# Performance work log

Measured on AMD Instinct MI355X. Metric: run time of the kernel, lower is better.

## Reference

```python
import jax, jax.numpy as jnp
import numpy as np

D = 1024      # config.input_dim
H = 16        # config.num_heads
EPS = 1e-6    # layernorm epsilon


def setup_inputs() -> dict:
    key = jax.random.key(0)
    ks = jax.random.split(key, 12)
    B, S = 4, 2048
    s = 1.0 / np.sqrt(D)
    return {
        "Q": jax.random.normal(ks[0], (B, S, D), jnp.float32),
        "K": jax.random.normal(ks[1], (B, S, D), jnp.float32),
        "V": jax.random.normal(ks[2], (B, S, D), jnp.float32),
        "Wq": jax.random.normal(ks[3], (D, D), jnp.float32) * s,
        "bq": jnp.zeros((D,), jnp.float32),
        "Wk": jax.random.normal(ks[4], (D, D), jnp.float32) * s,
        "bk": jnp.zeros((D,), jnp.float32),
        "Wv": jax.random.normal(ks[5], (D, D), jnp.float32) * s,
        "bv": jnp.zeros((D,), jnp.float32),
        "Wo": jax.random.normal(ks[6], (D, D), jnp.float32) * s,
        "bo": jnp.zeros((D,), jnp.float32),
        "gamma": jnp.ones((D,), jnp.float32),
        "beta": jnp.zeros((D,), jnp.float32),
    }


def _layernorm(x, gamma, beta):
    mu = jnp.mean(x, axis=-1, keepdims=True)
    var = jnp.mean(jnp.square(x - mu), axis=-1, keepdims=True)
    return (x - mu) * jax.lax.rsqrt(var + EPS) * gamma + beta


def reference(Q, K, V, Wq, bq, Wk, bk, Wv, bv, Wo, bo, gamma, beta):
    # Type == 'D': pre-norm projections, causal MHA (no 1/sqrt(d) scaling,
    # faithful to source), out projection, residual. Dropout = identity (eval).
    B, S, _ = Q.shape
    dh = D // H
    clone_Q = Q
    q = _layernorm(Q, gamma, beta) @ Wq + bq
    k = _layernorm(K, gamma, beta) @ Wk + bk
    v = _layernorm(V, gamma, beta) @ Wv + bv
    # [B, S, D] -> [B, H, S, dh]
    q = q.reshape(B, S, H, dh).transpose(0, 2, 1, 3)
    k = k.reshape(B, S, H, dh).transpose(0, 2, 1, 3)
    v = v.reshape(B, S, H, dh).transpose(0, 2, 1, 3)
    score = jnp.einsum("bhsd,bhtd->bhst", q, k)  # [B, H, S, S]
    causal = jnp.tril(jnp.ones((S, S), bool))
    score = jnp.where(causal, score, -jnp.inf)
    attn = jax.nn.softmax(score, axis=-1)
    out = jnp.einsum("bhst,bhtd->bhsd", attn, v)  # [B, H, S, dh]
    out = out.transpose(0, 2, 1, 3).reshape(B, S, D)
    return clone_Q + (out @ Wo + bo)
```

## Files before the change

kernel.cpp:

```cpp
#include <hip/hip_runtime.h>
#include <hip/hip_bf16.h>

typedef __attribute__((ext_vector_type(8))) __bf16 bf16x8;
typedef __attribute__((ext_vector_type(4))) float f32x4;

union BF8U { uint4 u; bf16x8 b; };

static __device__ __forceinline__ unsigned short f2bf(float f){
  union { float f; unsigned int u; } a; a.f = f;
  unsigned int u = a.u;
  return (unsigned short)((u + 0x7fffu + ((u >> 16) & 1u)) >> 16);
}

static __device__ __forceinline__ bf16x8 ld_bf8(const unsigned short* p){
  BF8U u; u.u = *reinterpret_cast<const uint4*>(p); return u.b;
}

static __device__ __forceinline__ f32x4 mfma16(bf16x8 a, bf16x8 b, f32x4 c){
  return __builtin_amdgcn_mfma_f32_16x16x32_bf16(a, b, c, 0, 0, 0);
}

static __device__ __forceinline__ void gl_lds16(const unsigned short* g, unsigned short* l){
  __builtin_amdgcn_global_load_lds(
      (const __attribute__((address_space(1))) unsigned int*)g,
      (__attribute__((address_space(3))) unsigned int*)l, 16, 0, 0);
}

__global__ __launch_bounds__(256) void ln_kernel(const float* __restrict__ X,
    const float* __restrict__ gamma, const float* __restrict__ beta,
    unsigned short* __restrict__ out)
{
  const int row = blockIdx.x;
  const int t = threadIdx.x;
  const float4 x = reinterpret_cast<const float4*>(X + (size_t)row*1024)[t];
  float s  = x.x + x.y + x.z + x.w;
  float ss = x.x*x.x + x.y*x.y + x.z*x.z + x.w*x.w;
  for (int off = 1; off < 64; off <<= 1){
    s  += __shfl_xor(s, off);
    ss += __shfl_xor(ss, off);
  }
  __shared__ float red[8];
  const int wv = t >> 6;
  if ((t & 63) == 0){ red[wv] = s; red[4 + wv] = ss; }
  __syncthreads();
  s  = red[0] + red[1] + red[2] + red[3];
  ss = red[4] + red[5] + red[6] + red[7];
  const float mu   = s * (1.0f/1024.0f);
  const float var  = ss * (1.0f/1024.0f) - mu*mu;
  const float rstd = rsqrtf(var + 1e-6f);
  const float4 gm = reinterpret_cast<const float4*>(gamma)[t];
  const float4 bt = reinterpret_cast<const float4*>(beta)[t];
  unsigned short pk[4];
  pk[0] = f2bf((x.x - mu)*rstd*gm.x + bt.x);
  pk[1] = f2bf((x.y - mu)*rstd*gm.y + bt.y);
  pk[2] = f2bf((x.z - mu)*rstd*gm.z + bt.z);
  pk[3] = f2bf((x.w - mu)*rstd*gm.w + bt.w);
  *reinterpret_cast<uint2*>(out + (size_t)row*1024 + t*4) = *reinterpret_cast<uint2*>(pk);
}

__global__ __launch_bounds__(256) void wt_kernel(const float* __restrict__ W,
    unsigned short* __restrict__ Wt)
{
  __shared__ unsigned short tile[64][72];
  const int t = threadIdx.x;
  const int bk = ((int)blockIdx.x >> 4) * 64;
  const int bn = ((int)blockIdx.x & 15) * 64;
  {
    const int kr = t >> 2, nc0 = (t & 3) * 16;
    const float4* src = reinterpret_cast<const float4*>(W + (size_t)(bk + kr)*1024 + bn + nc0);
    for (int q = 0; q < 4; ++q){
      float4 vv = src[q];
      tile[kr][nc0 + q*4 + 0] = f2bf(vv.x);
      tile[kr][nc0 + q*4 + 1] = f2bf(vv.y);
      tile[kr][nc0 + q*4 + 2] = f2bf(vv.z);
      tile[kr][nc0 + q*4 + 3] = f2bf(vv.w);
    }
  }
  __syncthreads();
  {
    const int nr = t >> 2, kc0 = (t & 3) * 16;
    unsigned short outv[16];
    for (int j = 0; j < 16; ++j) outv[j] = tile[kc0 + j][nr];
    uint4* dst = reinterpret_cast<uint4*>(Wt + (size_t)(bn + nr)*1024 + bk + kc0);
    dst[0] = reinterpret_cast<uint4*>(outv)[0];
    dst[1] = reinterpret_cast<uint4*>(outv)[1];
  }
}

template<int MODE>
__global__ __launch_bounds__(256) void gemm_kernel(
    const unsigned short* __restrict__ A,
    const unsigned short* __restrict__ Bt,
    const float* __restrict__ bias,
    const float* __restrict__ residual,
    unsigned short* __restrict__ outb,
    float* __restrict__ outf)
{
  __shared__ unsigned short a_lds[128][64];
  __shared__ unsigned short b_lds[128][64];
  const int t = threadIdx.x;
  const int lane = t & 63;
  const int w = t >> 6;
  const int g = lane >> 4, c = lane & 15;
  const int bm = (int)blockIdx.x >> 3, bn = (int)blockIdx.x & 7;
  const int wr = w >> 1, wc = w & 1;
  const int row0 = bm * 128, col0 = bn * 128;

  f32x4 acc[4][4];
  const f32x4 fz = {0.f, 0.f, 0.f, 0.f};
  for (int i = 0; i < 4; ++i) for (int j = 0; j < 4; ++j) acc[i][j] = fz;

  for (int kb = 0; kb < 1024; kb += 64){
    for (int i = 0; i < 4; ++i){
      const int cid = t + i*256;
      const int r = cid >> 3, ch = cid & 7;
      const int chs = (ch ^ (r & 7)) * 8;
      gl_lds16(&A [(size_t)(row0 + r)*1024 + kb + chs], &a_lds[0][0] + cid*8);
      gl_lds16(&Bt[(size_t)(col0 + r)*1024 + kb + chs], &b_lds[0][0] + cid*8);
    }
    __syncthreads();
    bf16x8 af[4][2], bfr[4][2];
    for (int mt = 0; mt < 4; ++mt)
      for (int kc = 0; kc < 2; ++kc){
        const int R = wr*64 + mt*16 + c;
        af[mt][kc] = ld_bf8(&a_lds[R][((kc*4 + g) ^ (R & 7))*8]);
      }
    for (int nt = 0; nt < 4; ++nt)
      for (int kc = 0; kc < 2; ++kc){
        const int R = wc*64 + nt*16 + c;
        bfr[nt][kc] = ld_bf8(&b_lds[R][((kc*4 + g) ^ (R & 7))*8]);
      }
    for (int kc = 0; kc < 2; ++kc)
      for (int mt = 0; mt < 4; ++mt)
        for (int nt = 0; nt < 4; ++nt)
          acc[mt][nt] = mfma16(af[mt][kc], bfr[nt][kc], acc[mt][nt]);
    __syncthreads();
  }

  for (int mt = 0; mt < 4; ++mt){
    for (int nt = 0; nt < 4; ++nt){
      const int gcol = col0 + wc*64 + nt*16 + c;
      const float bv = bias[gcol];
      if (MODE == 2){
        const int grow0 = row0 + wr*64 + mt*16 + g*4;
        const int bidx = grow0 >> 11, s0 = grow0 & 2047;
        const int hh = gcol >> 6, d = gcol & 63;
        unsigned short pk[4];
        for (int r = 0; r < 4; ++r) pk[r] = f2bf(acc[mt][nt][r] + bv);
        *reinterpret_cast<uint2*>(&outb[((size_t)((bidx*16 + hh)*64 + d))*2048 + s0]) =
          *reinterpret_cast<uint2*>(pk);
      } else {
        for (int r = 0; r < 4; ++r){
          const int grow = row0 + wr*64 + mt*16 + g*4 + r;
          float v = acc[mt][nt][r] + bv;
          if (MODE == 0){
            const int bidx = grow >> 11, s = grow & 2047;
            const int hh = gcol >> 6, d = gcol & 63;
            outb[((size_t)(bidx*16 + hh)*2048 + s)*64 + d] = f2bf(v);
          } else {
            const size_t idx = (size_t)grow*1024 + gcol;
            outf[idx] = v + residual[idx];
          }
        }
      }
    }
  }
}

__global__ __launch_bounds__(256) void attn_kernel(
    const unsigned short* __restrict__ qg,
    const unsigned short* __restrict__ kg,
    const unsigned short* __restrict__ vtg,
    unsigned short* __restrict__ og)
{
  __shared__ unsigned short k_lds[64][64];
  __shared__ unsigned short vt_lds[64][64];
  __shared__ unsigned short p_lds[4][32][72];
  const int t = threadIdx.x;
  const int lane = t & 63;
  const int w = t >> 6;
  const int g = lane >> 4, c = lane & 15;
  const int bh = (int)blockIdx.x & 63;
  const int p  = (int)blockIdx.x >> 6;
  const size_t base = (size_t)bh * 2048 * 64;
  const int bidx = bh >> 4, hh = bh & 15;
  const float NEG = -__builtin_inff();
  const f32x4 fz = {0.f,0.f,0.f,0.f};

  for (int half = 0; half < 2; ++half){
    const int qb = half ? (15 - p) : p;
    const int qw = qb*128 + w*32;

    bf16x8 qf[2][2];
    for (int mi = 0; mi < 2; ++mi)
      for (int kc = 0; kc < 2; ++kc)
        qf[mi][kc] = ld_bf8(&qg[base + (size_t)(qw + mi*16 + c)*64 + kc*32 + g*8]);

    f32x4 o_acc[4][2];
    for (int i = 0; i < 4; ++i) for (int j = 0; j < 2; ++j) o_acc[i][j] = fz;
    float m_run[2] = {NEG, NEG};
    float l_run[2] = {0.f, 0.f};

    const int nkv = qb*2 + 2;
    for (int kvt = 0; kvt < nkv; ++kvt){
      const int kv0 = kvt * 64;
      for (int i = 0; i < 2; ++i){
        const int cid = t + i*256;
        const int r = cid >> 3, ch = cid & 7;
        const int chs = (ch ^ (r & 7)) * 8;
        gl_lds16(&kg [base + (size_t)(kv0 + r)*64 + chs], &k_lds[0][0]  + cid*8);
        gl_lds16(&vtg[base + (size_t)r*2048 + kv0 + chs], &vt_lds[0][0] + cid*8);
      }
      __syncthreads();

      if (kv0 <= qw + 31){
        bf16x8 kf[4][2];
        for (int ni = 0; ni < 4; ++ni)
          for (int kc = 0; kc < 2; ++kc){
            const int R = ni*16 + c;
            kf[ni][kc] = ld_bf8(&k_lds[R][((kc*4 + g) ^ (R & 7))*8]);
          }
        f32x4 st[4][2];
        for (int i = 0; i < 4; ++i) for (int j = 0; j < 2; ++j) st[i][j] = fz;
        __builtin_amdgcn_s_setprio(1);
        for (int kc = 0; kc < 2; ++kc)
          for (int ni = 0; ni < 4; ++ni)
            for (int mi = 0; mi < 2; ++mi)
              st[ni][mi] = mfma16(kf[ni][kc], qf[mi][kc], st[ni][mi]);
        __builtin_amdgcn_s_setprio(0);

        const bool need_mask = (kv0 + 63 > qw);
        for (int mi = 0; mi < 2; ++mi){
          const int qglob = qw + mi*16 + c;
          float tmax = NEG;
          if (need_mask){
            for (int ni = 0; ni < 4; ++ni)
              for (int r = 0; r < 4; ++r){
                const int kvglob = kv0 + ni*16 + g*4 + r;
                float sv = (kvglob <= qglob) ? st[ni][mi][r] : NEG;
                st[ni][mi][r] = sv;
                tmax = fmaxf(tmax, sv);
              }
          } else {
            for (int ni = 0; ni < 4; ++ni)
              for (int r = 0; r < 4; ++r)
                tmax = fmaxf(tmax, st[ni][mi][r]);
          }
          tmax = fmaxf(tmax, __shfl_xor(tmax, 16));
          tmax = fmaxf(tmax, __shfl_xor(tmax, 32));
          const float m_new = fmaxf(m_run[mi], tmax);
          const float alpha = __expf(m_run[mi] - m_new);
          float tsum = 0.f;
          for (int ni = 0; ni < 4; ++ni)
            for (int r = 0; r < 4; ++r){
              const float pe = __expf(st[ni][mi][r] - m_new);
              st[ni][mi][r] = pe;
              tsum += pe;
            }
          tsum += __shfl_xor(tsum, 16);
          tsum += __shfl_xor(tsum, 32);
          l_run[mi] = l_run[mi]*alpha + tsum;
          m_run[mi] = m_new;
          for (int ni = 0; ni < 4; ++ni){
            o_acc[ni][mi][0] *= alpha; o_acc[ni][mi][1] *= alpha;
            o_acc[ni][mi][2] *= alpha; o_acc[ni][mi][3] *= alpha;
          }
          for (int ni = 0; ni < 4; ++ni){
            unsigned short pk[4];
            pk[0] = f2bf(st[ni][mi][0]); pk[1] = f2bf(st[ni][mi][1]);
            pk[2] = f2bf(st[ni][mi][2]); pk[3] = f2bf(st[ni][mi][3]);
            *reinterpret_cast<uint2*>(&p_lds[w][mi*16 + c][ni*16 + g*4]) =
              *reinterpret_cast<uint2*>(pk);
          }
        }

        bf16x8 vf[4][2], pf[2][2];
        for (int ni = 0; ni < 4; ++ni)
          for (int kc = 0; kc < 2; ++kc){
            const int R = ni*16 + c;
            vf[ni][kc] = ld_bf8(&vt_lds[R][((kc*4 + g) ^ (R & 7))*8]);
          }
        for (int kc = 0; kc < 2; ++kc)
          for (int mi = 0; mi < 2; ++mi)
            pf[kc][mi] = ld_bf8(&p_lds[w][mi*16 + c][kc*32 + g*8]);
        __builtin_amdgcn_s_setprio(1);
        for (int kc = 0; kc < 2; ++kc)
          for (int ni = 0; ni < 4; ++ni)
            for (int mi = 0; mi < 2; ++mi)
              o_acc[ni][mi] = mfma16(vf[ni][kc], pf[kc][mi], o_acc[ni][mi]);
        __builtin_amdgcn_s_setprio(0);
      }
      __syncthreads();
    }

    for (int mi = 0; mi < 2; ++mi){
      const float invl = 1.0f / l_run[mi];
      const int s = qw + mi*16 + c;
      const size_t obase = ((size_t)(bidx*2048 + s))*1024 + hh*64;
      for (int ni = 0; ni < 4; ++ni){
        unsigned short pk[4];
        pk[0] = f2bf(o_acc[ni][mi][0]*invl);
        pk[1] = f2bf(o_acc[ni][mi][1]*invl);
        pk[2] = f2bf(o_acc[ni][mi][2]*invl);
        pk[3] = f2bf(o_acc[ni][mi][3]*invl);
        *reinterpret_cast<uint2*>(&og[obase + ni*16 + g*4]) =
          *reinterpret_cast<uint2*>(pk);
      }
    }
  }
}

extern "C" void kernel_launch(void* const* d_in, const int* in_sizes, int n_in,
                              void* d_out, int out_size, void* d_ws, size_t ws_size,
                              hipStream_t stream)
{
  (void)in_sizes; (void)n_in; (void)out_size;
  const float* Q  = (const float*)d_in[0];
  const float* K  = (const float*)d_in[1];
  const float* V  = (const float*)d_in[2];
  const float* Wq = (const float*)d_in[3];
  const float* bq = (const float*)d_in[4];
  const float* Wk = (const float*)d_in[5];
  const float* bk = (const float*)d_in[6];
  const float* Wv = (const float*)d_in[7];
  const float* bv = (const float*)d_in[8];
  const float* Wo = (const float*)d_in[9];
  const float* bo = (const float*)d_in[10];
  const float* gamma = (const float*)d_in[11];
  const float* beta  = (const float*)d_in[12];

  const size_t MB = 1024ull*1024ull;
  if (ws_size < 104*MB) return;
  char* ws = (char*)d_ws;
  unsigned short* lnQ = (unsigned short*)(ws + 0*MB);
  unsigned short* lnK = (unsigned short*)(ws + 16*MB);
  unsigned short* lnV = (unsigned short*)(ws + 32*MB);
  unsigned short* attn_out = lnQ;
  unsigned short* WtQ = (unsigned short*)(ws + 48*MB);
  unsigned short* WtK = (unsigned short*)(ws + 50*MB);
  unsigned short* WtV = (unsigned short*)(ws + 52*MB);
  unsigned short* WtO = (unsigned short*)(ws + 54*MB);
  unsigned short* qb  = (unsigned short*)(ws + 56*MB);
  unsigned short* kb  = (unsigned short*)(ws + 72*MB);
  unsigned short* vtb = (unsigned short*)(ws + 88*MB);
  float* out = (float*)d_out;

  wt_kernel<<<256, 256, 0, stream>>>(Wq, WtQ);
  wt_kernel<<<256, 256, 0, stream>>>(Wk, WtK);
  wt_kernel<<<256, 256, 0, stream>>>(Wv, WtV);
  wt_kernel<<<256, 256, 0, stream>>>(Wo, WtO);
  ln_kernel<<<8192, 256, 0, stream>>>(Q, gamma, beta, lnQ);
  ln_kernel<<<8192, 256, 0, stream>>>(K, gamma, beta, lnK);
  ln_kernel<<<8192, 256, 0, stream>>>(V, gamma, beta, lnV);
  gemm_kernel<0><<<512, 256, 0, stream>>>(lnQ, WtQ, bq, nullptr, qb,  nullptr);
  gemm_kernel<0><<<512, 256, 0, stream>>>(lnK, WtK, bk, nullptr, kb,  nullptr);
  gemm_kernel<2><<<512, 256, 0, stream>>>(lnV, WtV, bv, nullptr, vtb, nullptr);
  attn_kernel<<<512, 256, 0, stream>>>(qb, kb, vtb, attn_out);
  gemm_kernel<1><<<512, 256, 0, stream>>>(attn_out, WtO, bo, Q, nullptr, out);
}
```

Measured before the change: 378.3 us.

## Merge prep and QKV launches, retile attention to 8 waves with deferred rescale

Folds the three layernorm launches and four weight transposes into one prep kernel, and the three QKV projections into a single 1536-block GEMM launch. The goal is to cut launch overhead and fill the GPU better. Attention moves to 512-thread blocks where each wave owns 16 query rows instead of 32, which reduces register pressure. Softmax pre-scales Q by log2(e) to use exp2, and skips the running-max rescale while the max grows by no more than a threshold. f2bf becomes a native cast. Deferring the rescale allows larger exponents before overflow, and halving each wave's query rows loses some K/V fragment reuse per wave.

Result: faster. 336.9 us (-10.9%).

```diff
diff --git a/kernel.cpp b/kernel.cpp
--- a/kernel.cpp
+++ b/kernel.cpp
@@ -7,9 +7,8 @@
 union BF8U { uint4 u; bf16x8 b; };
 
 static __device__ __forceinline__ unsigned short f2bf(float f){
-  union { float f; unsigned int u; } a; a.f = f;
-  unsigned int u = a.u;
-  return (unsigned short)((u + 0x7fffu + ((u >> 16) & 1u)) >> 16);
+  __bf16 h = (__bf16)f;
+  return *reinterpret_cast<unsigned short*>(&h);
 }
 
 static __device__ __forceinline__ bf16x8 ld_bf8(const unsigned short* p){
@@ -26,74 +25,168 @@
       (__attribute__((address_space(3))) unsigned int*)l, 16, 0, 0);
 }
 
-__global__ __launch_bounds__(256) void ln_kernel(const float* __restrict__ X,
+__global__ __launch_bounds__(256) void prep_kernel(
+    const float* __restrict__ Q, const float* __restrict__ K, const float* __restrict__ V,
     const float* __restrict__ gamma, const float* __restrict__ beta,
-    unsigned short* __restrict__ out)
+    unsigned short* __restrict__ lnQ, unsigned short* __restrict__ lnK,
+    unsigned short* __restrict__ lnV,
+    const float* __restrict__ Wq, const float* __restrict__ Wk,
+    const float* __restrict__ Wv, const float* __restrict__ Wo,
+    unsigned short* __restrict__ WtQ, unsigned short* __restrict__ WtK,
+    unsigned short* __restrict__ WtV, unsigned short* __restrict__ WtO)
 {
-  const int row = blockIdx.x;
+  __shared__ __align__(16) unsigned short smem[64*72];
+  const int bid = (int)blockIdx.x;
   const int t = threadIdx.x;
-  const float4 x = reinterpret_cast<const float4*>(X + (size_t)row*1024)[t];
-  float s  = x.x + x.y + x.z + x.w;
-  float ss = x.x*x.x + x.y*x.y + x.z*x.z + x.w*x.w;
-  for (int off = 1; off < 64; off <<= 1){
-    s  += __shfl_xor(s, off);
-    ss += __shfl_xor(ss, off);
-  }
-  __shared__ float red[8];
-  const int wv = t >> 6;
-  if ((t & 63) == 0){ red[wv] = s; red[4 + wv] = ss; }
-  __syncthreads();
-  s  = red[0] + red[1] + red[2] + red[3];
-  ss = red[4] + red[5] + red[6] + red[7];
-  const float mu   = s * (1.0f/1024.0f);
-  const float var  = ss * (1.0f/1024.0f) - mu*mu;
-  const float rstd = rsqrtf(var + 1e-6f);
-  const float4 gm = reinterpret_cast<const float4*>(gamma)[t];
-  const float4 bt = reinterpret_cast<const float4*>(beta)[t];
-  unsigned short pk[4];
-  pk[0] = f2bf((x.x - mu)*rstd*gm.x + bt.x);
-  pk[1] = f2bf((x.y - mu)*rstd*gm.y + bt.y);
-  pk[2] = f2bf((x.z - mu)*rstd*gm.z + bt.z);
-  pk[3] = f2bf((x.w - mu)*rstd*gm.w + bt.w);
-  *reinterpret_cast<uint2*>(out + (size_t)row*1024 + t*4) = *reinterpret_cast<uint2*>(pk);
-}
-
-__global__ __launch_bounds__(256) void wt_kernel(const float* __restrict__ W,
-    unsigned short* __restrict__ Wt)
+  if (bid < 24576){
+    const int sel = bid >> 13;
+    const int row = bid & 8191;
+    const float* X = sel==0 ? Q : sel==1 ? K : V;
+    unsigned short* out = sel==0 ? lnQ : sel==1 ? lnK : lnV;
+    float* red = reinterpret_cast<float*>(smem);
+    const float4 x = reinterpret_cast<const float4*>(X + (size_t)row*1024)[t];
+    float s  = x.x + x.y + x.z + x.w;
+    float ss = x.x*x.x + x.y*x.y + x.z*x.z + x.w*x.w;
+    for (int off = 1; off < 64; off <<= 1){
+      s  += __shfl_xor(s, off);
+      ss += __shfl_xor(ss, off);
+    }
+    const int wv = t >> 6;
+    if ((t & 63) == 0){ red[wv] = s; red[4 + wv] = ss; }
+    __syncthreads();
+    s  = red[0] + red[1] + red[2] + red[3];
+    ss = red[4] + red[5] + red[6] + red[7];
+    const float mu   = s * (1.0f/1024.0f);
+    const float var  = ss * (1.0f/1024.0f) - mu*mu;
+    const float rstd = rsqrtf(var + 1e-6f);
+    const float4 gm = reinterpret_cast<const float4*>(gamma)[t];
+    const float4 bt = reinterpret_cast<const float4*>(beta)[t];
+    unsigned short pk[4];
+    pk[0] = f2bf((x.x - mu)*rstd*gm.x + bt.x);
+    pk[1] = f2bf((x.y - mu)*rstd*gm.y + bt.y);
+    pk[2] = f2bf((x.z - mu)*rstd*gm.z + bt.z);
+    pk[3] = f2bf((x.w - mu)*rstd*gm.w + bt.w);
+    *reinterpret_cast<uint2*>(out + (size_t)row*1024 + t*4) = *reinterpret_cast<uint2*>(pk);
+  } else {
+    const int wid = bid - 24576;
+    const int wsel = wid >> 8;
+    const float* W = wsel==0 ? Wq : wsel==1 ? Wk : wsel==2 ? Wv : Wo;
+    unsigned short* Wt = wsel==0 ? WtQ : wsel==1 ? WtK : wsel==2 ? WtV : WtO;
+    unsigned short (*tile)[72] = reinterpret_cast<unsigned short(*)[72]>(smem);
+    const int tb = wid & 255;
+    const int bk = (tb >> 4) * 64;
+    const int bn = (tb & 15) * 64;
+    {
+      const int kr = t >> 2, nc0 = (t & 3) * 16;
+      const float4* src = reinterpret_cast<const float4*>(W + (size_t)(bk + kr)*1024 + bn + nc0);
+      for (int q = 0; q < 4; ++q){
+        float4 vv = src[q];
+        tile[kr][nc0 + q*4 + 0] = f2bf(vv.x);
+        tile[kr][nc0 + q*4 + 1] = f2bf(vv.y);
+        tile[kr][nc0 + q*4 + 2] = f2bf(vv.z);
+        tile[kr][nc0 + q*4 + 3] = f2bf(vv.w);
+      }
+    }
+    __syncthreads();
+    {
+      const int nr = t >> 2, kc0 = (t & 3) * 16;
+      unsigned short outv[16];
+      for (int j = 0; j < 16; ++j) outv[j] = tile[kc0 + j][nr];
+      uint4* dst = reinterpret_cast<uint4*>(Wt + (size_t)(bn + nr)*1024 + bk + kc0);
+      dst[0] = reinterpret_cast<uint4*>(outv)[0];
+      dst[1] = reinterpret_cast<uint4*>(outv)[1];
+    }
+  }
+}
+
+__global__ __launch_bounds__(256) void qkv_kernel(
+    const unsigned short* __restrict__ lnQ, const unsigned short* __restrict__ lnK,
+    const unsigned short* __restrict__ lnV,
+    const unsigned short* __restrict__ WtQ, const unsigned short* __restrict__ WtK,
+    const unsigned short* __restrict__ WtV,
+    const float* __restrict__ bq, const float* __restrict__ bk,
+    const float* __restrict__ bv,
+    unsigned short* __restrict__ qb, unsigned short* __restrict__ kb,
+    unsigned short* __restrict__ vtb)
 {
-  __shared__ unsigned short tile[64][72];
+  __shared__ unsigned short a_lds[128][64];
+  __shared__ unsigned short b_lds[128][64];
+  const int bid = (int)blockIdx.x;
+  const int which = bid >> 9;
+  const int inner = bid & 511;
+  const unsigned short* A  = which==0 ? lnQ : which==1 ? lnK : lnV;
+  const unsigned short* Bt = which==0 ? WtQ : which==1 ? WtK : WtV;
+  const float* bias = which==0 ? bq : which==1 ? bk : bv;
+
   const int t = threadIdx.x;
-  const int bk = ((int)blockIdx.x >> 4) * 64;
-  const int bn = ((int)blockIdx.x & 15) * 64;
-  {
-    const int kr = t >> 2, nc0 = (t & 3) * 16;
-    const float4* src = reinterpret_cast<const float4*>(W + (size_t)(bk + kr)*1024 + bn + nc0);
-    for (int q = 0; q < 4; ++q){
-      float4 vv = src[q];
-      tile[kr][nc0 + q*4 + 0] = f2bf(vv.x);
-      tile[kr][nc0 + q*4 + 1] = f2bf(vv.y);
-      tile[kr][nc0 + q*4 + 2] = f2bf(vv.z);
-      tile[kr][nc0 + q*4 + 3] = f2bf(vv.w);
-    }
-  }
-  __syncthreads();
-  {
-    const int nr = t >> 2, kc0 = (t & 3) * 16;
-    unsigned short outv[16];
-    for (int j = 0; j < 16; ++j) outv[j] = tile[kc0 + j][nr];
-    uint4* dst = reinterpret_cast<uint4*>(Wt + (size_t)(bn + nr)*1024 + bk + kc0);
-    dst[0] = reinterpret_cast<uint4*>(outv)[0];
-    dst[1] = reinterpret_cast<uint4*>(outv)[1];
-  }
-}
-
-template<int MODE>
-__global__ __launch_bounds__(256) void gemm_kernel(
+  const int lane = t & 63;
+  const int w = t >> 6;
+  const int g = lane >> 4, c = lane & 15;
+  const int bm = inner >> 3, bn = inner & 7;
+  const int wr = w >> 1, wc = w & 1;
+  const int row0 = bm * 128, col0 = bn * 128;
+
+  f32x4 acc[4][4];
+  const f32x4 fz = {0.f, 0.f, 0.f, 0.f};
+  for (int i = 0; i < 4; ++i) for (int j = 0; j < 4; ++j) acc[i][j] = fz;
+
+  for (int kb_ = 0; kb_ < 1024; kb_ += 64){
+    for (int i = 0; i < 4; ++i){
+      const int cid = t + i*256;
+      const int r = cid >> 3, ch = cid & 7;
+      const int chs = (ch ^ (r & 7)) * 8;
+      gl_lds16(&A [(size_t)(row0 + r)*1024 + kb_ + chs], &a_lds[0][0] + cid*8);
+      gl_lds16(&Bt[(size_t)(col0 + r)*1024 + kb_ + chs], &b_lds[0][0] + cid*8);
+    }
+    __syncthreads();
+    bf16x8 af[4][2], bfr[4][2];
+    for (int mt = 0; mt < 4; ++mt)
+      for (int kc = 0; kc < 2; ++kc){
+        const int R = wr*64 + mt*16 + c;
+        af[mt][kc] = ld_bf8(&a_lds[R][((kc*4 + g) ^ (R & 7))*8]);
+      }
+    for (int nt = 0; nt < 4; ++nt)
+      for (int kc = 0; kc < 2; ++kc){
+        const int R = wc*64 + nt*16 + c;
+        bfr[nt][kc] = ld_bf8(&b_lds[R][((kc*4 + g) ^ (R & 7))*8]);
+      }
+    for (int kc = 0; kc < 2; ++kc)
+      for (int mt = 0; mt < 4; ++mt)
+        for (int nt = 0; nt < 4; ++nt)
+          acc[mt][nt] = mfma16(af[mt][kc], bfr[nt][kc], acc[mt][nt]);
+    __syncthreads();
+  }
+
+  const float scale = (which == 0) ? 1.4426950408889634f : 1.0f;
+  unsigned short* outb = which==0 ? qb : kb;
+  for (int mt = 0; mt < 4; ++mt){
+    for (int nt = 0; nt < 4; ++nt){
+      const int gcol = col0 + wc*64 + nt*16 + c;
+      const float bv_ = bias[gcol];
+      const int hh = gcol >> 6, d = gcol & 63;
+      if (which == 2){
+        const int grow0 = row0 + wr*64 + mt*16 + g*4;
+        const int bidx = grow0 >> 11, s0 = grow0 & 2047;
+        unsigned short pk[4];
+        for (int r = 0; r < 4; ++r) pk[r] = f2bf(acc[mt][nt][r] + bv_);
+        *reinterpret_cast<uint2*>(&vtb[((size_t)((bidx*16 + hh)*64 + d))*2048 + s0]) =
+          *reinterpret_cast<uint2*>(pk);
+      } else {
+        for (int r = 0; r < 4; ++r){
+          const int grow = row0 + wr*64 + mt*16 + g*4 + r;
+          const int bidx = grow >> 11, s = grow & 2047;
+          outb[((size_t)(bidx*16 + hh)*2048 + s)*64 + d] = f2bf((acc[mt][nt][r] + bv_)*scale);
+        }
+      }
+    }
+  }
+}
+
+__global__ __launch_bounds__(256) void ogemm_kernel(
     const unsigned short* __restrict__ A,
     const unsigned short* __restrict__ Bt,
     const float* __restrict__ bias,
     const float* __restrict__ residual,
-    unsigned short* __restrict__ outb,
     float* __restrict__ outf)
 {
   __shared__ unsigned short a_lds[128][64];
@@ -110,13 +203,13 @@
   const f32x4 fz = {0.f, 0.f, 0.f, 0.f};
   for (int i = 0; i < 4; ++i) for (int j = 0; j < 4; ++j) acc[i][j] = fz;
 
-  for (int kb = 0; kb < 1024; kb += 64){
+  for (int kb_ = 0; kb_ < 1024; kb_ += 64){
     for (int i = 0; i < 4; ++i){
       const int cid = t + i*256;
       const int r = cid >> 3, ch = cid & 7;
       const int chs = (ch ^ (r & 7)) * 8;
-      gl_lds16(&A [(size_t)(row0 + r)*1024 + kb + chs], &a_lds[0][0] + cid*8);
-      gl_lds16(&Bt[(size_t)(col0 + r)*1024 + kb + chs], &b_lds[0][0] + cid*8);
+      gl_lds16(&A [(size_t)(row0 + r)*1024 + kb_ + chs], &a_lds[0][0] + cid*8);
+      gl_lds16(&Bt[(size_t)(col0 + r)*1024 + kb_ + chs], &b_lds[0][0] + cid*8);
     }
     __syncthreads();
     bf16x8 af[4][2], bfr[4][2];
@@ -140,34 +233,17 @@
   for (int mt = 0; mt < 4; ++mt){
     for (int nt = 0; nt < 4; ++nt){
       const int gcol = col0 + wc*64 + nt*16 + c;
-      const float bv = bias[gcol];
-      if (MODE == 2){
-        const int grow0 = row0 + wr*64 + mt*16 + g*4;
-        const int bidx = grow0 >> 11, s0 = grow0 & 2047;
-        const int hh = gcol >> 6, d = gcol & 63;
-        unsigned short pk[4];
-        for (int r = 0; r < 4; ++r) pk[r] = f2bf(acc[mt][nt][r] + bv);
-        *reinterpret_cast<uint2*>(&outb[((size_t)((bidx*16 + hh)*64 + d))*2048 + s0]) =
-          *reinterpret_cast<uint2*>(pk);
-      } else {
-        for (int r = 0; r < 4; ++r){
-          const int grow = row0 + wr*64 + mt*16 + g*4 + r;
-          float v = acc[mt][nt][r] + bv;
-          if (MODE == 0){
-            const int bidx = grow >> 11, s = grow & 2047;
-            const int hh = gcol >> 6, d = gcol & 63;
-            outb[((size_t)(bidx*16 + hh)*2048 + s)*64 + d] = f2bf(v);
-          } else {
-            const size_t idx = (size_t)grow*1024 + gcol;
-            outf[idx] = v + residual[idx];
-          }
-        }
-      }
-    }
-  }
-}
-
-__global__ __launch_bounds__(256) void attn_kernel(
+      const float bv_ = bias[gcol];
+      for (int r = 0; r < 4; ++r){
+        const int grow = row0 + wr*64 + mt*16 + g*4 + r;
+        const size_t idx = (size_t)grow*1024 + gcol;
+        outf[idx] = acc[mt][nt][r] + bv_ + residual[idx];
+      }
+    }
+  }
+}
+
+__global__ __launch_bounds__(512, 4) void attn_kernel(
     const unsigned short* __restrict__ qg,
     const unsigned short* __restrict__ kg,
     const unsigned short* __restrict__ vtg,
@@ -175,7 +251,7 @@
 {
   __shared__ unsigned short k_lds[64][64];
   __shared__ unsigned short vt_lds[64][64];
-  __shared__ unsigned short p_lds[4][32][72];
+  __shared__ unsigned short p_lds[8][16][72];
   const int t = threadIdx.x;
   const int lane = t & 63;
   const int w = t >> 6;
@@ -187,125 +263,115 @@
   const float NEG = -__builtin_inff();
   const f32x4 fz = {0.f,0.f,0.f,0.f};
 
+  const int sr = t >> 3, sch = t & 7;
+  const int schs = (sch ^ (sr & 7)) * 8;
+
   for (int half = 0; half < 2; ++half){
-    const int qb = half ? (15 - p) : p;
-    const int qw = qb*128 + w*32;
-
-    bf16x8 qf[2][2];
-    for (int mi = 0; mi < 2; ++mi)
-      for (int kc = 0; kc < 2; ++kc)
-        qf[mi][kc] = ld_bf8(&qg[base + (size_t)(qw + mi*16 + c)*64 + kc*32 + g*8]);
-
-    f32x4 o_acc[4][2];
-    for (int i = 0; i < 4; ++i) for (int j = 0; j < 2; ++j) o_acc[i][j] = fz;
-    float m_run[2] = {NEG, NEG};
-    float l_run[2] = {0.f, 0.f};
-
-    const int nkv = qb*2 + 2;
+    const int qb_ = half ? (15 - p) : p;
+    const int qw = qb_*128 + w*16;
+
+    bf16x8 qf[2];
+    for (int kc = 0; kc < 2; ++kc)
+      qf[kc] = ld_bf8(&qg[base + (size_t)(qw + c)*64 + kc*32 + g*8]);
+
+    f32x4 o_acc[4];
+    for (int i = 0; i < 4; ++i) o_acc[i] = fz;
+    float m_run = NEG, l_run = 0.f;
+
+    const int nkv = qb_*2 + 2;
     for (int kvt = 0; kvt < nkv; ++kvt){
       const int kv0 = kvt * 64;
-      for (int i = 0; i < 2; ++i){
-        const int cid = t + i*256;
-        const int r = cid >> 3, ch = cid & 7;
-        const int chs = (ch ^ (r & 7)) * 8;
-        gl_lds16(&kg [base + (size_t)(kv0 + r)*64 + chs], &k_lds[0][0]  + cid*8);
-        gl_lds16(&vtg[base + (size_t)r*2048 + kv0 + chs], &vt_lds[0][0] + cid*8);
-      }
+      gl_lds16(&kg [base + (size_t)(kv0 + sr)*64 + schs], &k_lds[0][0]  + t*8);
+      gl_lds16(&vtg[base + (size_t)sr*2048 + kv0 + schs], &vt_lds[0][0] + t*8);
       __syncthreads();
 
-      if (kv0 <= qw + 31){
+      if (kv0 <= qw + 15){
         bf16x8 kf[4][2];
         for (int ni = 0; ni < 4; ++ni)
           for (int kc = 0; kc < 2; ++kc){
             const int R = ni*16 + c;
             kf[ni][kc] = ld_bf8(&k_lds[R][((kc*4 + g) ^ (R & 7))*8]);
           }
-        f32x4 st[4][2];
-        for (int i = 0; i < 4; ++i) for (int j = 0; j < 2; ++j) st[i][j] = fz;
+        f32x4 st[4];
+        for (int i = 0; i < 4; ++i) st[i] = fz;
         __builtin_amdgcn_s_setprio(1);
         for (int kc = 0; kc < 2; ++kc)
           for (int ni = 0; ni < 4; ++ni)
-            for (int mi = 0; mi < 2; ++mi)
-              st[ni][mi] = mfma16(kf[ni][kc], qf[mi][kc], st[ni][mi]);
+            st[ni] = mfma16(kf[ni][kc], qf[kc], st[ni]);
         __builtin_amdgcn_s_setprio(0);
 
-        const bool need_mask = (kv0 + 63 > qw);
-        for (int mi = 0; mi < 2; ++mi){
-          const int qglob = qw + mi*16 + c;
-          float tmax = NEG;
-          if (need_mask){
-            for (int ni = 0; ni < 4; ++ni)
-              for (int r = 0; r < 4; ++r){
-                const int kvglob = kv0 + ni*16 + g*4 + r;
-                float sv = (kvglob <= qglob) ? st[ni][mi][r] : NEG;
-                st[ni][mi][r] = sv;
-                tmax = fmaxf(tmax, sv);
-              }
-          } else {
-            for (int ni = 0; ni < 4; ++ni)
-              for (int r = 0; r < 4; ++r)
-                tmax = fmaxf(tmax, st[ni][mi][r]);
-          }
-          tmax = fmaxf(tmax, __shfl_xor(tmax, 16));
-          tmax = fmaxf(tmax, __shfl_xor(tmax, 32));
-          const float m_new = fmaxf(m_run[mi], tmax);
-          const float alpha = __expf(m_run[mi] - m_new);
-          float tsum = 0.f;
+        const int qglob = qw + c;
+        float tmax = NEG;
+        if (kv0 + 63 > qw){
           for (int ni = 0; ni < 4; ++ni)
             for (int r = 0; r < 4; ++r){
-              const float pe = __expf(st[ni][mi][r] - m_new);
-              st[ni][mi][r] = pe;
-              tsum += pe;
+              const int kvglob = kv0 + ni*16 + g*4 + r;
+              float sv = (kvglob <= qglob) ? st[ni][r] : NEG;
+              st[ni][r] = sv;
+              tmax = fmaxf(tmax, sv);
             }
-          tsum += __shfl_xor(tsum, 16);
-          tsum += __shfl_xor(tsum, 32);
-          l_run[mi] = l_run[mi]*alpha + tsum;
-          m_run[mi] = m_new;
+        } else {
+          for (int ni = 0; ni < 4; ++ni)
+            for (int r = 0; r < 4; ++r)
+              tmax = fmaxf(tmax, st[ni][r]);
+        }
+        tmax = fmaxf(tmax, __shfl_xor(tmax, 16));
+        tmax = fmaxf(tmax, __shfl_xor(tmax, 32));
+
+        const bool defer = __all(tmax - m_run <= 11.5f);
+        if (!defer){
+          const float m_new = fmaxf(m_run, tmax);
+          const float alpha = __builtin_amdgcn_exp2f(m_run - m_new);
+          m_run = m_new;
+          l_run *= alpha;
           for (int ni = 0; ni < 4; ++ni){
-            o_acc[ni][mi][0] *= alpha; o_acc[ni][mi][1] *= alpha;
-            o_acc[ni][mi][2] *= alpha; o_acc[ni][mi][3] *= alpha;
-          }
-          for (int ni = 0; ni < 4; ++ni){
-            unsigned short pk[4];
-            pk[0] = f2bf(st[ni][mi][0]); pk[1] = f2bf(st[ni][mi][1]);
-            pk[2] = f2bf(st[ni][mi][2]); pk[3] = f2bf(st[ni][mi][3]);
-            *reinterpret_cast<uint2*>(&p_lds[w][mi*16 + c][ni*16 + g*4]) =
-              *reinterpret_cast<uint2*>(pk);
+            o_acc[ni][0] *= alpha; o_acc[ni][1] *= alpha;
+            o_acc[ni][2] *= alpha; o_acc[ni][3] *= alpha;
           }
         }
-
-        bf16x8 vf[4][2], pf[2][2];
+        float tsum = 0.f;
+        for (int ni = 0; ni < 4; ++ni){
+          unsigned short pk[4];
+          for (int r = 0; r < 4; ++r){
+            const float pe = __builtin_amdgcn_exp2f(st[ni][r] - m_run);
+            tsum += pe;
+            pk[r] = f2bf(pe);
+          }
+          *reinterpret_cast<uint2*>(&p_lds[w][c][ni*16 + g*4]) =
+            *reinterpret_cast<uint2*>(pk);
+        }
+        tsum += __shfl_xor(tsum, 16);
+        tsum += __shfl_xor(tsum, 32);
+        l_run += tsum;
+
+        bf16x8 vf[4][2], pf[2];
         for (int ni = 0; ni < 4; ++ni)
           for (int kc = 0; kc < 2; ++kc){
             const int R = ni*16 + c;
             vf[ni][kc] = ld_bf8(&vt_lds[R][((kc*4 + g) ^ (R & 7))*8]);
           }
         for (int kc = 0; kc < 2; ++kc)
-          for (int mi = 0; mi < 2; ++mi)
-            pf[kc][mi] = ld_bf8(&p_lds[w][mi*16 + c][kc*32 + g*8]);
+          pf[kc] = ld_bf8(&p_lds[w][c][kc*32 + g*8]);
         __builtin_amdgcn_s_setprio(1);
         for (int kc = 0; kc < 2; ++kc)
           for (int ni = 0; ni < 4; ++ni)
-            for (int mi = 0; mi < 2; ++mi)
-              o_acc[ni][mi] = mfma16(vf[ni][kc], pf[kc][mi], o_acc[ni][mi]);
+            o_acc[ni] = mfma16(vf[ni][kc], pf[kc], o_acc[ni]);
         __builtin_amdgcn_s_setprio(0);
       }
       __syncthreads();
     }
 
-    for (int mi = 0; mi < 2; ++mi){
-      const float invl = 1.0f / l_run[mi];
-      const int s = qw + mi*16 + c;
-      const size_t obase = ((size_t)(bidx*2048 + s))*1024 + hh*64;
-      for (int ni = 0; ni < 4; ++ni){
-        unsigned short pk[4];
-        pk[0] = f2bf(o_acc[ni][mi][0]*invl);
-        pk[1] = f2bf(o_acc[ni][mi][1]*invl);
-        pk[2] = f2bf(o_acc[ni][mi][2]*invl);
-        pk[3] = f2bf(o_acc[ni][mi][3]*invl);
-        *reinterpret_cast<uint2*>(&og[obase + ni*16 + g*4]) =
-          *reinterpret_cast<uint2*>(pk);
-      }
+    const float invl = 1.0f / l_run;
+    const int s = qw + c;
+    const size_t obase = ((size_t)(bidx*2048 + s))*1024 + hh*64;
+    for (int ni = 0; ni < 4; ++ni){
+      unsigned short pk[4];
+      pk[0] = f2bf(o_acc[ni][0]*invl);
+      pk[1] = f2bf(o_acc[ni][1]*invl);
+      pk[2] = f2bf(o_acc[ni][2]*invl);
+      pk[3] = f2bf(o_acc[ni][3]*invl);
+      *reinterpret_cast<uint2*>(&og[obase + ni*16 + g*4]) =
+        *reinterpret_cast<uint2*>(pk);
     }
   }
 }
@@ -345,16 +411,10 @@
   unsigned short* vtb = (unsigned short*)(ws + 88*MB);
   float* out = (float*)d_out;
 
-  wt_kernel<<<256, 256, 0, stream>>>(Wq, WtQ);
-  wt_kernel<<<256, 256, 0, stream>>>(Wk, WtK);
-  wt_kernel<<<256, 256, 0, stream>>>(Wv, WtV);
-  wt_kernel<<<256, 256, 0, stream>>>(Wo, WtO);
-  ln_kernel<<<8192, 256, 0, stream>>>(Q, gamma, beta, lnQ);
-  ln_kernel<<<8192, 256, 0, stream>>>(K, gamma, beta, lnK);
-  ln_kernel<<<8192, 256, 0, stream>>>(V, gamma, beta, lnV);
-  gemm_kernel<0><<<512, 256, 0, stream>>>(lnQ, WtQ, bq, nullptr, qb,  nullptr);
-  gemm_kernel<0><<<512, 256, 0, stream>>>(lnK, WtK, bk, nullptr, kb,  nullptr);
-  gemm_kernel<2><<<512, 256, 0, stream>>>(lnV, WtV, bv, nullptr, vtb, nullptr);
-  attn_kernel<<<512, 256, 0, stream>>>(qb, kb, vtb, attn_out);
-  gemm_kernel<1><<<512, 256, 0, stream>>>(attn_out, WtO, bo, Q, nullptr, out);
-}
+  prep_kernel<<<25600, 256, 0, stream>>>(Q, K, V, gamma, beta, lnQ, lnK, lnV,
+                                         Wq, Wk, Wv, Wo, WtQ, WtK, WtV, WtO);
+  qkv_kernel<<<1536, 256, 0, stream>>>(lnQ, lnK, lnV, WtQ, WtK, WtV,
+                                       bq, bk, bv, qb, kb, vtb);
+  attn_kernel<<<512, 512, 0, stream>>>(qb, kb, vtb, attn_out);
+  ogemm_kernel<<<512, 256, 0, stream>>>(attn_out, WtO, bo, Q, out);
+}
```
